# Optimization experiments

Hardware: AMD Instinct MI355X
Metric: run time of the kernel (lower is better)

## Reference

```python
import jax, jax.numpy as jnp
import numpy as np

HIDDEN = 1024
QUERY = 1024
NUM_EXPERTS = 64
TOP_K = 2

def setup_inputs() -> dict:
    key = jax.random.key(0)
    k1, k2, k3 = jax.random.split(key, 3)
    B, total, num_tokens = 8, 128, 576
    vis_emb = jax.random.normal(k1, (total, num_tokens, HIDDEN), dtype=jnp.float32)
    query_emb = jax.random.normal(k2, (B, QUERY), dtype=jnp.float32)
    # nn.Linear default init scale ~ 1/sqrt(fan_in)
    W_gate = jax.random.normal(k3, (NUM_EXPERTS, HIDDEN + QUERY), dtype=jnp.float32) / np.sqrt(HIDDEN + QUERY)
    return {"vis_emb": vis_emb, "query_emb": query_emb, "W_gate": W_gate}

def reference(vis_emb, query_emb, W_gate):
    # Faithful to: cat([vis, query_expanded], -1) @ W.T, but expressed as two
    # split matmuls (identical math, avoids materializing the concat).
    total = vis_emb.shape[0]
    B = query_emb.shape[0]
    repeat = total // B
    W_vis = W_gate[:, :HIDDEN]    # [E, H]
    W_qry = W_gate[:, HIDDEN:]    # [E, Q]
    vis_logits = jnp.einsum('nth,eh->nte', vis_emb, W_vis)          # [total, T, E]
    qry_logits = jnp.einsum('bq,eq->be', query_emb, W_qry)          # [B, E]
    qry_logits = jnp.repeat(qry_logits, repeat, axis=0)[:, None, :]  # [total, 1, E]
    gate_logits = vis_logits + qry_logits                            # [total, T, E]
    gate_scores = jax.nn.softmax(gate_logits, axis=-1)
    topk_scores, topk_idx = jax.lax.top_k(gate_scores, TOP_K)
    return (topk_scores, topk_idx, gate_scores, gate_logits)
```

## Files before the change

### kernel.cpp

```cpp
#include <hip/hip_runtime.h>
#include <math.h>

#define HIDDEN    1024
#define NEXP      64
#define MTILE     64
#define KSTEP     64

#define WT_OFF 0
#define QL_OFF 65536

#define OUT_TKS 0
#define OUT_TKI 147456
#define OUT_GS  294912
#define OUT_GL  5013504

typedef const __attribute__((address_space(1))) void* gas_p;
typedef __attribute__((address_space(3))) void* las_p;

__device__ __forceinline__ void g2lds16(const float* g, float* l) {
  __builtin_amdgcn_global_load_lds((gas_p)(const void*)g, (las_p)(void*)l, 16, 0, 0);
}

__global__ __launch_bounds__(256) void prep_kernel(
    const float* __restrict__ query_emb, const float* __restrict__ W_gate,
    float* __restrict__ ws) {
  const int bid = blockIdx.x;
  const int tid = threadIdx.x;
  if (bid < 256) {
    const int idx = bid * 256 + tid;
    const int k = idx >> 6, e = idx & 63;
    ws[WT_OFF + idx] = W_gate[e * 2048 + k];
  } else {
    const int b = bid - 256;
    const int e = tid >> 2, q = tid & 3;
    const float* qp = query_emb + b * 1024 + q * 256;
    const float* wp = W_gate + e * 2048 + 1024 + q * 256;
    float s = 0.f;
    #pragma unroll 4
    for (int j = 0; j < 256; j += 4) {
      const float4 a = *(const float4*)(qp + j);
      const float4 w = *(const float4*)(wp + j);
      s += a.x * w.x + a.y * w.y + a.z * w.z + a.w * w.w;
    }
    s += __shfl_xor(s, 1);
    s += __shfl_xor(s, 2);
    if (q == 0) ws[QL_OFF + b * 64 + e] = s;
  }
}

__global__ __launch_bounds__(256) void router_main(
    const float* __restrict__ vis, const float* __restrict__ ws,
    float* __restrict__ out) {
  __shared__ __align__(16) float As[KSTEP * 64];
  __shared__ __align__(16) float Ws[KSTEP * 64];
  const int tid = threadIdx.x;
  const int tx = tid & 15, ty = tid >> 4;
  const int lane = tid & 63, wv = tid >> 6;
  const long base = (long)blockIdx.x * MTILE;
  const float* Wt = ws + WT_OFF;

  float acc[4][4] = {};

  for (int k0 = 0; k0 < HIDDEN; k0 += KSTEP) {
    __syncthreads();
    {
      const float* gw = Wt + k0 * 64 + wv * 1024 + lane * 4;
      float* lw = &Ws[wv * 1024];
      #pragma unroll
      for (int c = 0; c < 4; ++c)
        g2lds16(gw + c * 256, lw + c * 256);
    }
    #pragma unroll
    for (int p = 0; p < 4; ++p) {
      const int ii = p * 256 + tid;
      const int t = ii >> 4, kg = ii & 15;
      const float4 v = *(const float4*)(vis + (base + t) * 1024 + k0 + kg * 4);
      const int w0 = kg * 256 + (t ^ (kg * 4));
      As[w0]       = v.x;
      As[w0 + 64]  = v.y;
      As[w0 + 128] = v.z;
      As[w0 + 192] = v.w;
    }
    __syncthreads();
    #pragma unroll 8
    for (int k = 0; k < KSTEP; ++k) {
      const float4 a = *(const float4*)&As[k * 64 + ((ty * 4) ^ ((k >> 2) * 4))];
      const float4 b = *(const float4*)&Ws[k * 64 + tx * 4];
      acc[0][0] += a.x * b.x; acc[0][1] += a.x * b.y; acc[0][2] += a.x * b.z; acc[0][3] += a.x * b.w;
      acc[1][0] += a.y * b.x; acc[1][1] += a.y * b.y; acc[1][2] += a.y * b.z; acc[1][3] += a.y * b.w;
      acc[2][0] += a.z * b.x; acc[2][1] += a.z * b.y; acc[2][2] += a.z * b.z; acc[2][3] += a.z * b.w;
      acc[3][0] += a.w * b.x; acc[3][1] += a.w * b.y; acc[3][2] += a.w * b.z; acc[3][3] += a.w * b.w;
    }
  }

  const int bq = (int)(base / 9216);
  const float4 qv = *(const float4*)(ws + QL_OFF + bq * 64 + tx * 4);

  float* out_tks = out + OUT_TKS;
  float* out_tki = out + OUT_TKI;
  float* out_gs  = out + OUT_GS;
  float* out_gl  = out + OUT_GL;

  #pragma unroll
  for (int i = 0; i < 4; ++i) {
    const long tok = base + ty * 4 + i;
    const float l0 = acc[i][0] + qv.x;
    const float l1 = acc[i][1] + qv.y;
    const float l2 = acc[i][2] + qv.z;
    const float l3 = acc[i][3] + qv.w;
    *(float4*)(out_gl + tok * 64 + tx * 4) = make_float4(l0, l1, l2, l3);

    float m = fmaxf(fmaxf(l0, l1), fmaxf(l2, l3));
    #pragma unroll
    for (int msk = 1; msk < 16; msk <<= 1) m = fmaxf(m, __shfl_xor(m, msk));

    const float e0 = expf(l0 - m), e1 = expf(l1 - m), e2 = expf(l2 - m), e3 = expf(l3 - m);
    float ssum = e0 + e1 + e2 + e3;
    #pragma unroll
    for (int msk = 1; msk < 16; msk <<= 1) ssum += __shfl_xor(ssum, msk);
    const float inv = 1.0f / ssum;
    const float s0 = e0 * inv, s1 = e1 * inv, s2 = e2 * inv, s3 = e3 * inv;
    *(float4*)(out_gs + tok * 64 + tx * 4) = make_float4(s0, s1, s2, s3);

    float v1 = s0, v2 = s1; int i1 = tx * 4, i2 = tx * 4 + 1;
    if (s1 > v1) { v2 = v1; i2 = i1; v1 = s1; i1 = tx * 4 + 1; }
    if (s2 > v1)      { v2 = v1; i2 = i1; v1 = s2; i1 = tx * 4 + 2; }
    else if (s2 > v2) { v2 = s2; i2 = tx * 4 + 2; }
    if (s3 > v1)      { v2 = v1; i2 = i1; v1 = s3; i1 = tx * 4 + 3; }
    else if (s3 > v2) { v2 = s3; i2 = tx * 4 + 3; }

    #pragma unroll
    for (int msk = 1; msk < 16; msk <<= 1) {
      const float w1 = __shfl_xor(v1, msk), w2 = __shfl_xor(v2, msk);
      const int   j1 = __shfl_xor(i1, msk), j2 = __shfl_xor(i2, msk);
      const bool wfirst = (w1 > v1) || (w1 == v1 && j1 < i1);
      if (wfirst) {
        const bool vsec = (v1 > w2) || (v1 == w2 && i1 < j2);
        v2 = vsec ? v1 : w2; i2 = vsec ? i1 : j2;
        v1 = w1; i1 = j1;
      } else {
        const bool wsec = (w1 > v2) || (w1 == v2 && j1 < i2);
        if (wsec) { v2 = w1; i2 = j1; }
      }
    }
    if (tx == 0) {
      *(float2*)(out_tks + tok * 2) = make_float2(v1, v2);
      *(float2*)(out_tki + tok * 2) = make_float2((float)i1, (float)i2);
    }
  }
}

extern "C" void kernel_launch(void* const* d_in, const int* in_sizes, int n_in,
                              void* d_out, int out_size, void* d_ws, size_t ws_size,
                              hipStream_t stream) {
  const float* vis   = (const float*)d_in[0];
  const float* query = (const float*)d_in[1];
  const float* wg    = (const float*)d_in[2];
  float* ws  = (float*)d_ws;
  float* o   = (float*)d_out;
  hipLaunchKernelGGL(prep_kernel, dim3(264), dim3(256), 0, stream, query, wg, ws);
  hipLaunchKernelGGL(router_main, dim3(1152), dim3(256), 0, stream, vis, ws, o);
}
```

Baseline: 507.7 us.

## Use single-wave blocks with 8x8 register tiles and register prefetch

The main GEMM block shrinks from 256 to 64 threads, each computing an 8x8 output tile instead of 4x4, which raises arithmetic per LDS read. The K chunk drops to 32, and the next chunk of vis and W is prefetched into registers while the current one is computed. Because a block is now a single wavefront, the barriers are removed. The async global-to-LDS loads are dropped. This costs much higher register pressure and far fewer waves in flight (1152 single-wave blocks), which may limit how much memory latency is hidden on a kernel that mostly streams vis from memory.

```diff
diff --git a/kernel.cpp b/kernel.cpp
--- a/kernel.cpp
+++ b/kernel.cpp
@@ -1,10 +1,10 @@
 #include <hip/hip_runtime.h>
 #include <math.h>
 
-#define HIDDEN    1024
-#define NEXP      64
-#define MTILE     64
-#define KSTEP     64
+#define HIDDEN 1024
+#define NEXP   64
+#define MT     64
+#define KC     32
 
 #define WT_OFF 0
 #define QL_OFF 65536
@@ -13,13 +13,6 @@
 #define OUT_TKI 147456
 #define OUT_GS  294912
 #define OUT_GL  5013504
-
-typedef const __attribute__((address_space(1))) void* gas_p;
-typedef __attribute__((address_space(3))) void* las_p;
-
-__device__ __forceinline__ void g2lds16(const float* g, float* l) {
-  __builtin_amdgcn_global_load_lds((gas_p)(const void*)g, (las_p)(void*)l, 16, 0, 0);
-}
 
 __global__ __launch_bounds__(256) void prep_kernel(
     const float* __restrict__ query_emb, const float* __restrict__ W_gate,
@@ -48,53 +41,74 @@
   }
 }
 
-__global__ __launch_bounds__(256) void router_main(
+__global__ __launch_bounds__(64, 2) void router_main(
     const float* __restrict__ vis, const float* __restrict__ ws,
     float* __restrict__ out) {
-  __shared__ __align__(16) float As[KSTEP * 64];
-  __shared__ __align__(16) float Ws[KSTEP * 64];
+  __shared__ __align__(16) float As[KC * 64];
+  __shared__ __align__(16) float Ws[KC * 64];
   const int tid = threadIdx.x;
-  const int tx = tid & 15, ty = tid >> 4;
-  const int lane = tid & 63, wv = tid >> 6;
-  const long base = (long)blockIdx.x * MTILE;
+  const int ec  = tid & 7;
+  const int r   = tid >> 3;
+  const int k4  = tid & 7;
+  const long base = (long)blockIdx.x * MT;
   const float* Wt = ws + WT_OFF;
+  const float* arow = vis + base * HIDDEN;
 
-  float acc[4][4] = {};
+  float acc[8][8] = {};
 
-  for (int k0 = 0; k0 < HIDDEN; k0 += KSTEP) {
-    __syncthreads();
-    {
-      const float* gw = Wt + k0 * 64 + wv * 1024 + lane * 4;
-      float* lw = &Ws[wv * 1024];
-      #pragma unroll
-      for (int c = 0; c < 4; ++c)
-        g2lds16(gw + c * 256, lw + c * 256);
+  float4 pfa[8];
+  float4 pfb[8];
+  #pragma unroll
+  for (int p = 0; p < 8; ++p)
+    pfa[p] = *(const float4*)(arow + (p * 8 + r) * HIDDEN + k4 * 4);
+  #pragma unroll
+  for (int i = 0; i < 8; ++i)
+    pfb[i] = *(const float4*)(Wt + i * 256 + tid * 4);
+
+  for (int c = 0; c < 32; ++c) {
+    #pragma unroll
+    for (int p = 0; p < 8; ++p) {
+      const int t = p * 8 + r;
+      const int w0 = (k4 * 4) * 64 + (t ^ (k4 * 4));
+      As[w0]       = pfa[p].x;
+      As[w0 + 64]  = pfa[p].y;
+      As[w0 + 128] = pfa[p].z;
+      As[w0 + 192] = pfa[p].w;
     }
     #pragma unroll
-    for (int p = 0; p < 4; ++p) {
-      const int ii = p * 256 + tid;
-      const int t = ii >> 4, kg = ii & 15;
-      const float4 v = *(const float4*)(vis + (base + t) * 1024 + k0 + kg * 4);
-      const int w0 = kg * 256 + (t ^ (kg * 4));
-      As[w0]       = v.x;
-      As[w0 + 64]  = v.y;
-      As[w0 + 128] = v.z;
-      As[w0 + 192] = v.w;
-    }
-    __syncthreads();
-    #pragma unroll 8
-    for (int k = 0; k < KSTEP; ++k) {
-      const float4 a = *(const float4*)&As[k * 64 + ((ty * 4) ^ ((k >> 2) * 4))];
-      const float4 b = *(const float4*)&Ws[k * 64 + tx * 4];
-      acc[0][0] += a.x * b.x; acc[0][1] += a.x * b.y; acc[0][2] += a.x * b.z; acc[0][3] += a.x * b.w;
-      acc[1][0] += a.y * b.x; acc[1][1] += a.y * b.y; acc[1][2] += a.y * b.z; acc[1][3] += a.y * b.w;
-      acc[2][0] += a.z * b.x; acc[2][1] += a.z * b.y; acc[2][2] += a.z * b.z; acc[2][3] += a.z * b.w;
-      acc[3][0] += a.w * b.x; acc[3][1] += a.w * b.y; acc[3][2] += a.w * b.z; acc[3][3] += a.w * b.w;
+    for (int i = 0; i < 8; ++i)
+      *(float4*)&Ws[i * 256 + tid * 4] = pfb[i];
+
+    const int kn = (c < 31) ? (c + 1) * KC : 0;
+    #pragma unroll
+    for (int p = 0; p < 8; ++p)
+      pfa[p] = *(const float4*)(arow + (p * 8 + r) * HIDDEN + kn + k4 * 4);
+    #pragma unroll
+    for (int i = 0; i < 8; ++i)
+      pfb[i] = *(const float4*)(Wt + kn * 64 + i * 256 + tid * 4);
+
+    #pragma unroll 4
+    for (int k = 0; k < KC; ++k) {
+      const int sw = k & 28;
+      const int ai = k * 64 + ((r * 8) ^ sw);
+      const float4 a0 = *(const float4*)&As[ai];
+      const float4 a1 = *(const float4*)&As[ai ^ 4];
+      const float4 b0 = *(const float4*)&Ws[k * 64 + ec * 8];
+      const float4 b1 = *(const float4*)&Ws[k * 64 + ec * 8 + 4];
+      const float av[8] = {a0.x, a0.y, a0.z, a0.w, a1.x, a1.y, a1.z, a1.w};
+      const float bv[8] = {b0.x, b0.y, b0.z, b0.w, b1.x, b1.y, b1.z, b1.w};
+      #pragma unroll
+      for (int i = 0; i < 8; ++i)
+        #pragma unroll
+        for (int j = 0; j < 8; ++j)
+          acc[i][j] += av[i] * bv[j];
     }
   }
 
-  const int bq = (int)(base / 9216);
-  const float4 qv = *(const float4*)(ws + QL_OFF + bq * 64 + tx * 4);
+  const int bq = blockIdx.x / 144;
+  const float4 qv0 = *(const float4*)(ws + QL_OFF + bq * 64 + ec * 8);
+  const float4 qv1 = *(const float4*)(ws + QL_OFF + bq * 64 + ec * 8 + 4);
+  const float ql[8] = {qv0.x, qv0.y, qv0.z, qv0.w, qv1.x, qv1.y, qv1.z, qv1.w};
 
   float* out_tks = out + OUT_TKS;
   float* out_tki = out + OUT_TKI;
@@ -102,35 +116,42 @@
   float* out_gl  = out + OUT_GL;
 
   #pragma unroll
-  for (int i = 0; i < 4; ++i) {
-    const long tok = base + ty * 4 + i;
-    const float l0 = acc[i][0] + qv.x;
-    const float l1 = acc[i][1] + qv.y;
-    const float l2 = acc[i][2] + qv.z;
-    const float l3 = acc[i][3] + qv.w;
-    *(float4*)(out_gl + tok * 64 + tx * 4) = make_float4(l0, l1, l2, l3);
+  for (int i = 0; i < 8; ++i) {
+    const long tok = base + r * 8 + i;
+    float l[8];
+    #pragma unroll
+    for (int j = 0; j < 8; ++j) l[j] = acc[i][j] + ql[j];
+    *(float4*)(out_gl + tok * 64 + ec * 8)     = make_float4(l[0], l[1], l[2], l[3]);
+    *(float4*)(out_gl + tok * 64 + ec * 8 + 4) = make_float4(l[4], l[5], l[6], l[7]);
 
-    float m = fmaxf(fmaxf(l0, l1), fmaxf(l2, l3));
+    float m = l[0];
     #pragma unroll
-    for (int msk = 1; msk < 16; msk <<= 1) m = fmaxf(m, __shfl_xor(m, msk));
+    for (int j = 1; j < 8; ++j) m = fmaxf(m, l[j]);
+    m = fmaxf(m, __shfl_xor(m, 1));
+    m = fmaxf(m, __shfl_xor(m, 2));
+    m = fmaxf(m, __shfl_xor(m, 4));
 
-    const float e0 = expf(l0 - m), e1 = expf(l1 - m), e2 = expf(l2 - m), e3 = expf(l3 - m);
-    float ssum = e0 + e1 + e2 + e3;
+    float s[8], ssum = 0.f;
     #pragma unroll
-    for (int msk = 1; msk < 16; msk <<= 1) ssum += __shfl_xor(ssum, msk);
+    for (int j = 0; j < 8; ++j) { s[j] = expf(l[j] - m); ssum += s[j]; }
+    ssum += __shfl_xor(ssum, 1);
+    ssum += __shfl_xor(ssum, 2);
+    ssum += __shfl_xor(ssum, 4);
     const float inv = 1.0f / ssum;
-    const float s0 = e0 * inv, s1 = e1 * inv, s2 = e2 * inv, s3 = e3 * inv;
-    *(float4*)(out_gs + tok * 64 + tx * 4) = make_float4(s0, s1, s2, s3);
+    #pragma unroll
+    for (int j = 0; j < 8; ++j) s[j] *= inv;
+    *(float4*)(out_gs + tok * 64 + ec * 8)     = make_float4(s[0], s[1], s[2], s[3]);
+    *(float4*)(out_gs + tok * 64 + ec * 8 + 4) = make_float4(s[4], s[5], s[6], s[7]);
 
-    float v1 = s0, v2 = s1; int i1 = tx * 4, i2 = tx * 4 + 1;
-    if (s1 > v1) { v2 = v1; i2 = i1; v1 = s1; i1 = tx * 4 + 1; }
-    if (s2 > v1)      { v2 = v1; i2 = i1; v1 = s2; i1 = tx * 4 + 2; }
-    else if (s2 > v2) { v2 = s2; i2 = tx * 4 + 2; }
-    if (s3 > v1)      { v2 = v1; i2 = i1; v1 = s3; i1 = tx * 4 + 3; }
-    else if (s3 > v2) { v2 = s3; i2 = tx * 4 + 3; }
-
+    float v1 = s[0], v2 = s[1]; int i1 = ec * 8, i2 = ec * 8 + 1;
+    if (s[1] > v1) { v2 = v1; i2 = i1; v1 = s[1]; i1 = ec * 8 + 1; }
     #pragma unroll
-    for (int msk = 1; msk < 16; msk <<= 1) {
+    for (int j = 2; j < 8; ++j) {
+      if (s[j] > v1)      { v2 = v1; i2 = i1; v1 = s[j]; i1 = ec * 8 + j; }
+      else if (s[j] > v2) { v2 = s[j]; i2 = ec * 8 + j; }
+    }
+    #pragma unroll
+    for (int msk = 1; msk < 8; msk <<= 1) {
       const float w1 = __shfl_xor(v1, msk), w2 = __shfl_xor(v2, msk);
       const int   j1 = __shfl_xor(i1, msk), j2 = __shfl_xor(i2, msk);
       const bool wfirst = (w1 > v1) || (w1 == v1 && j1 < i1);
@@ -143,7 +164,7 @@
         if (wsec) { v2 = w1; i2 = j1; }
       }
     }
-    if (tx == 0) {
+    if (ec == 0) {
       *(float2*)(out_tks + tok * 2) = make_float2(v1, v2);
       *(float2*)(out_tki + tok * 2) = make_float2((float)i1, (float)i2);
     }
@@ -159,5 +180,5 @@
   float* ws  = (float*)d_ws;
   float* o   = (float*)d_out;
   hipLaunchKernelGGL(prep_kernel, dim3(264), dim3(256), 0, stream, query, wg, ws);
-  hipLaunchKernelGGL(router_main, dim3(1152), dim3(256), 0, stream, vis, ws, o);
+  hipLaunchKernelGGL(router_main, dim3(1152), dim3(64), 0, stream, vis, ws, o);
 }
```

Measured after the change: 638.6 us. 25.8% more time.

## Replace FP32 FMA GEMM with split-fp16 MFMA emulation of fp32 precision

Applied to the files above, without the earlier changes.

Swaps the LDS-tiled scalar FP32 outer-product GEMM for MFMA 16x16x32 f16 instructions. Each operand is split into a high and a scaled low fp16 part, and three MFMAs per tile recover near-fp32 accuracy. Weights are pre-split and pre-swizzled into fragment order by the prep kernel. Vis rows are loaded straight from global memory into registers with one-step prefetch, and shared memory and barriers are removed. The cost is a 3x MFMA count and precision that depends on the fp16 range of the split. Because the kernel likely streams the ~300MB vis tensor, it may be memory-bound and gain less.

```diff
diff --git a/kernel.cpp b/kernel.cpp
--- a/kernel.cpp
+++ b/kernel.cpp
@@ -1,40 +1,46 @@
 #include <hip/hip_runtime.h>
 #include <math.h>
 
-#define HIDDEN    1024
-#define NEXP      64
-#define MTILE     64
-#define KSTEP     64
+#define HIDDEN 1024
 
-#define WT_OFF 0
-#define QL_OFF 65536
+typedef _Float16 half8 __attribute__((ext_vector_type(8)));
+typedef float floatx4 __attribute__((ext_vector_type(4)));
 
 #define OUT_TKS 0
 #define OUT_TKI 147456
 #define OUT_GS  294912
 #define OUT_GL  5013504
 
-typedef const __attribute__((address_space(1))) void* gas_p;
-typedef __attribute__((address_space(3))) void* las_p;
-
-__device__ __forceinline__ void g2lds16(const float* g, float* l) {
-  __builtin_amdgcn_global_load_lds((gas_p)(const void*)g, (las_p)(void*)l, 16, 0, 0);
-}
+#define QL_FOFF 65536
 
 __global__ __launch_bounds__(256) void prep_kernel(
     const float* __restrict__ query_emb, const float* __restrict__ W_gate,
     float* __restrict__ ws) {
-  const int bid = blockIdx.x;
-  const int tid = threadIdx.x;
-  if (bid < 256) {
-    const int idx = bid * 256 + tid;
-    const int k = idx >> 6, e = idx & 63;
-    ws[WT_OFF + idx] = W_gate[e * 2048 + k];
+  const int bid = blockIdx.x, tid = threadIdx.x;
+  if (bid < 64) {
+    _Float16* WH = (_Float16*)ws;
+    _Float16* WL = WH + 65536;
+    const int base = (bid * 256 + tid) * 4;
+    #pragma unroll
+    for (int u = 0; u < 4; ++u) {
+      const int idx = base + u;
+      const int j  = idx & 7;
+      const int L  = (idx >> 3) & 63;
+      const int nt = (idx >> 9) & 3;
+      const int c  = idx >> 11;
+      const int e  = nt * 16 + (L & 15);
+      const int k  = c * 32 + (L >> 4) * 8 + j;
+      const float w = W_gate[e * 2048 + k];
+      const _Float16 hi = (_Float16)w;
+      const float hif = (float)hi;
+      WH[idx] = hi;
+      WL[idx] = (_Float16)((w - hif) * 2048.0f);
+    }
   } else {
-    const int b = bid - 256;
-    const int e = tid >> 2, q = tid & 3;
-    const float* qp = query_emb + b * 1024 + q * 256;
-    const float* wp = W_gate + e * 2048 + 1024 + q * 256;
+    const int b = bid - 64;
+    const int e = tid >> 2, qq = tid & 3;
+    const float* qp = query_emb + b * 1024 + qq * 256;
+    const float* wp = W_gate + e * 2048 + 1024 + qq * 256;
     float s = 0.f;
     #pragma unroll 4
     for (int j = 0; j < 256; j += 4) {
@@ -44,57 +50,71 @@
     }
     s += __shfl_xor(s, 1);
     s += __shfl_xor(s, 2);
-    if (q == 0) ws[QL_OFF + b * 64 + e] = s;
+    if (qq == 0) ws[QL_FOFF + b * 64 + e] = s;
   }
 }
 
-__global__ __launch_bounds__(256) void router_main(
+__global__ __launch_bounds__(256, 3) void router_main(
     const float* __restrict__ vis, const float* __restrict__ ws,
     float* __restrict__ out) {
-  __shared__ __align__(16) float As[KSTEP * 64];
-  __shared__ __align__(16) float Ws[KSTEP * 64];
   const int tid = threadIdx.x;
-  const int tx = tid & 15, ty = tid >> 4;
-  const int lane = tid & 63, wv = tid >> 6;
-  const long base = (long)blockIdx.x * MTILE;
-  const float* Wt = ws + WT_OFF;
+  const int L  = tid & 63;
+  const int wv = tid >> 6;
+  const int m  = L & 15;
+  const int q  = L >> 4;
+  const long t0 = (long)blockIdx.x * 64 + wv * 16;
+  const _Float16* WH = (const _Float16*)ws;
+  const _Float16* WL = WH + 65536;
+  const float* QL = ws + QL_FOFF;
 
-  float acc[4][4] = {};
+  const float* ap = vis + (t0 + m) * HIDDEN + q * 8;
+  const int fo = L * 8;
 
-  for (int k0 = 0; k0 < HIDDEN; k0 += KSTEP) {
-    __syncthreads();
-    {
-      const float* gw = Wt + k0 * 64 + wv * 1024 + lane * 4;
-      float* lw = &Ws[wv * 1024];
-      #pragma unroll
-      for (int c = 0; c < 4; ++c)
-        g2lds16(gw + c * 256, lw + c * 256);
-    }
-    #pragma unroll
-    for (int p = 0; p < 4; ++p) {
-      const int ii = p * 256 + tid;
-      const int t = ii >> 4, kg = ii & 15;
-      const float4 v = *(const float4*)(vis + (base + t) * 1024 + k0 + kg * 4);
-      const int w0 = kg * 256 + (t ^ (kg * 4));
-      As[w0]       = v.x;
-      As[w0 + 64]  = v.y;
-      As[w0 + 128] = v.z;
-      As[w0 + 192] = v.w;
-    }
-    __syncthreads();
-    #pragma unroll 8
-    for (int k = 0; k < KSTEP; ++k) {
-      const float4 a = *(const float4*)&As[k * 64 + ((ty * 4) ^ ((k >> 2) * 4))];
-      const float4 b = *(const float4*)&Ws[k * 64 + tx * 4];
-      acc[0][0] += a.x * b.x; acc[0][1] += a.x * b.y; acc[0][2] += a.x * b.z; acc[0][3] += a.x * b.w;
-      acc[1][0] += a.y * b.x; acc[1][1] += a.y * b.y; acc[1][2] += a.y * b.z; acc[1][3] += a.y * b.w;
-      acc[2][0] += a.z * b.x; acc[2][1] += a.z * b.y; acc[2][2] += a.z * b.z; acc[2][3] += a.z * b.w;
-      acc[3][0] += a.w * b.x; acc[3][1] += a.w * b.y; acc[3][2] += a.w * b.z; acc[3][3] += a.w * b.w;
-    }
+  floatx4 acc[4], accx[4];
+  #pragma unroll
+  for (int nt = 0; nt < 4; ++nt) {
+    acc[nt]  = (floatx4){0.f, 0.f, 0.f, 0.f};
+    accx[nt] = (floatx4){0.f, 0.f, 0.f, 0.f};
   }
 
-  const int bq = (int)(base / 9216);
-  const float4 qv = *(const float4*)(ws + QL_OFF + bq * 64 + tx * 4);
+  float4 a0 = *(const float4*)ap;
+  float4 a1 = *(const float4*)(ap + 4);
+
+  for (int c = 0; c < 32; ++c) {
+    const float* apn = ap + ((c < 31) ? 32 : 0);
+    const float4 n0 = *(const float4*)apn;
+    const float4 n1 = *(const float4*)(apn + 4);
+
+    half8 ah, al;
+    {
+      const float av[8] = {a0.x, a0.y, a0.z, a0.w, a1.x, a1.y, a1.z, a1.w};
+      #pragma unroll
+      for (int j = 0; j < 8; ++j) {
+        const _Float16 h = (_Float16)av[j];
+        ah[j] = h;
+        al[j] = (_Float16)((av[j] - (float)h) * 2048.0f);
+      }
+    }
+
+    const _Float16* whp = WH + (c * 4) * 512 + fo;
+    const _Float16* wlp = WL + (c * 4) * 512 + fo;
+    #pragma unroll
+    for (int nt = 0; nt < 4; ++nt) {
+      const half8 wh = *(const half8*)(whp + nt * 512);
+      const half8 wl = *(const half8*)(wlp + nt * 512);
+      acc[nt]  = __builtin_amdgcn_mfma_f32_16x16x32_f16(ah, wh, acc[nt],  0, 0, 0);
+      accx[nt] = __builtin_amdgcn_mfma_f32_16x16x32_f16(ah, wl, accx[nt], 0, 0, 0);
+      accx[nt] = __builtin_amdgcn_mfma_f32_16x16x32_f16(al, wh, accx[nt], 0, 0, 0);
+    }
+
+    ap = apn;
+    a0 = n0; a1 = n1;
+  }
+
+  const int bq = blockIdx.x / 144;
+  float ql[4];
+  #pragma unroll
+  for (int nt = 0; nt < 4; ++nt) ql[nt] = QL[bq * 64 + nt * 16 + m];
 
   float* out_tks = out + OUT_TKS;
   float* out_tki = out + OUT_TKI;
@@ -103,31 +123,41 @@
 
   #pragma unroll
   for (int i = 0; i < 4; ++i) {
-    const long tok = base + ty * 4 + i;
-    const float l0 = acc[i][0] + qv.x;
-    const float l1 = acc[i][1] + qv.y;
-    const float l2 = acc[i][2] + qv.z;
-    const float l3 = acc[i][3] + qv.w;
-    *(float4*)(out_gl + tok * 64 + tx * 4) = make_float4(l0, l1, l2, l3);
+    const long tok = t0 + q * 4 + i;
+    float l[4];
+    #pragma unroll
+    for (int nt = 0; nt < 4; ++nt)
+      l[nt] = acc[nt][i] + accx[nt][i] * (1.0f / 2048.0f) + ql[nt];
+    #pragma unroll
+    for (int nt = 0; nt < 4; ++nt)
+      out_gl[tok * 64 + nt * 16 + m] = l[nt];
 
-    float m = fmaxf(fmaxf(l0, l1), fmaxf(l2, l3));
+    float mx = fmaxf(fmaxf(l[0], l[1]), fmaxf(l[2], l[3]));
+    mx = fmaxf(mx, __shfl_xor(mx, 1));
+    mx = fmaxf(mx, __shfl_xor(mx, 2));
+    mx = fmaxf(mx, __shfl_xor(mx, 4));
+    mx = fmaxf(mx, __shfl_xor(mx, 8));
+
+    float s[4], ssum = 0.f;
     #pragma unroll
-    for (int msk = 1; msk < 16; msk <<= 1) m = fmaxf(m, __shfl_xor(m, msk));
+    for (int nt = 0; nt < 4; ++nt) { s[nt] = expf(l[nt] - mx); ssum += s[nt]; }
+    ssum += __shfl_xor(ssum, 1);
+    ssum += __shfl_xor(ssum, 2);
+    ssum += __shfl_xor(ssum, 4);
+    ssum += __shfl_xor(ssum, 8);
+    const float inv = 1.0f / ssum;
+    #pragma unroll
+    for (int nt = 0; nt < 4; ++nt) s[nt] *= inv;
+    #pragma unroll
+    for (int nt = 0; nt < 4; ++nt)
+      out_gs[tok * 64 + nt * 16 + m] = s[nt];
 
-    const float e0 = expf(l0 - m), e1 = expf(l1 - m), e2 = expf(l2 - m), e3 = expf(l3 - m);
-    float ssum = e0 + e1 + e2 + e3;
-    #pragma unroll
-    for (int msk = 1; msk < 16; msk <<= 1) ssum += __shfl_xor(ssum, msk);
-    const float inv = 1.0f / ssum;
-    const float s0 = e0 * inv, s1 = e1 * inv, s2 = e2 * inv, s3 = e3 * inv;
-    *(float4*)(out_gs + tok * 64 + tx * 4) = make_float4(s0, s1, s2, s3);
-
-    float v1 = s0, v2 = s1; int i1 = tx * 4, i2 = tx * 4 + 1;
-    if (s1 > v1) { v2 = v1; i2 = i1; v1 = s1; i1 = tx * 4 + 1; }
-    if (s2 > v1)      { v2 = v1; i2 = i1; v1 = s2; i1 = tx * 4 + 2; }
-    else if (s2 > v2) { v2 = s2; i2 = tx * 4 + 2; }
-    if (s3 > v1)      { v2 = v1; i2 = i1; v1 = s3; i1 = tx * 4 + 3; }
-    else if (s3 > v2) { v2 = s3; i2 = tx * 4 + 3; }
+    float v1 = s[0], v2 = s[1]; int i1 = m, i2 = 16 + m;
+    if (s[1] > v1) { v2 = v1; i2 = i1; v1 = s[1]; i1 = 16 + m; }
+    if (s[2] > v1)      { v2 = v1; i2 = i1; v1 = s[2]; i1 = 32 + m; }
+    else if (s[2] > v2) { v2 = s[2]; i2 = 32 + m; }
+    if (s[3] > v1)      { v2 = v1; i2 = i1; v1 = s[3]; i1 = 48 + m; }
+    else if (s[3] > v2) { v2 = s[3]; i2 = 48 + m; }
 
     #pragma unroll
     for (int msk = 1; msk < 16; msk <<= 1) {
@@ -143,7 +173,7 @@
         if (wsec) { v2 = w1; i2 = j1; }
       }
     }
-    if (tx == 0) {
+    if (m == 0) {
       *(float2*)(out_tks + tok * 2) = make_float2(v1, v2);
       *(float2*)(out_tki + tok * 2) = make_float2((float)i1, (float)i2);
     }
@@ -156,8 +186,8 @@
   const float* vis   = (const float*)d_in[0];
   const float* query = (const float*)d_in[1];
   const float* wg    = (const float*)d_in[2];
-  float* ws  = (float*)d_ws;
-  float* o   = (float*)d_out;
-  hipLaunchKernelGGL(prep_kernel, dim3(264), dim3(256), 0, stream, query, wg, ws);
+  float* ws = (float*)d_ws;
+  float* o  = (float*)d_out;
+  hipLaunchKernelGGL(prep_kernel, dim3(72), dim3(256), 0, stream, query, wg, ws);
   hipLaunchKernelGGL(router_main, dim3(1152), dim3(256), 0, stream, vis, ws, o);
 }
```

Measured after the change: 495.6 us. 2.4% less time.
